# Performance work log

Measured on AMD Instinct MI355X. Metric: run time of the kernel, lower is better.

Reference implementation:

```python
import jax, jax.numpy as jnp
import numpy as np

_N = 262144  # horizon
_n = 64      # state dim
_m = 32      # observation dim


def setup_inputs() -> dict:
    key = jax.random.key(0)
    k1, k2, k3, k4 = jax.random.split(key, 4)
    # Scale so the closed-loop matrix M = A - L H is stable (spectral radius < 1);
    # otherwise the 262k-step recurrence overflows fp32.
    A = jax.random.normal(k1, (_n, _n), jnp.float32) * (0.7 / np.sqrt(_n))
    H = jax.random.normal(k2, (_m, _n), jnp.float32) * (1.0 / np.sqrt(_n))
    L = jax.random.normal(k3, (_n, _m), jnp.float32) * (0.1 / np.sqrt(_m))
    y = jax.random.normal(k4, (_m, _N), jnp.float32)
    return {"y": y, "A": A, "H": H, "L": L, "N": _N}


def reference(y, A, H, L, N):
    # xhat[k+1] = A xhat[k] + L (y[:,k] - H xhat[:,k]) = (A - L H) xhat[k] + L y[:,k]
    # yhat[:,k] = H xhat[:,k],  xhat[0] = 0
    M = A - L @ H  # (n, n) closed-loop transition
    x0 = jnp.zeros((A.shape[0],), dtype=A.dtype)

    def step(x, yk):
        yhat_k = H @ x          # emitted BEFORE the update (matches loop order)
        x_next = M @ x + L @ yk
        return x_next, yhat_k

    _, yhat = jax.lax.scan(step, x0, y.T[:N])  # yhat: (N, m)
    return yhat.T  # (m, N)
```

## Files before the change

### kernel.cpp

```cpp
#include <hip/hip_runtime.h>
#include <hip/hip_bf16.h>


#define NSTEP 262144
#define T 16
#define CCH (NSTEP / T)
#define KDIM (64 + 32 * T)
#define MOUT (32 * T)
#define NBLK 128
#define SB (CCH / NBLK)

typedef _Float16 f16;
typedef _Float16 f16x4 __attribute__((ext_vector_type(4)));
typedef _Float16 f16x8 __attribute__((ext_vector_type(8)));
typedef float f32x4 __attribute__((ext_vector_type(4)));


#define OFF_ZH 0
#define SZ_ZH  (CCH * KDIM / 2)
#define OFF_VT (OFF_ZH + SZ_ZH)
#define SZ_VT  (CCH * 64)
#define OFF_MP (OFF_VT + SZ_VT)
#define SZ_MP  (8 * 4096)
#define OFF_BO (OFF_MP + SZ_MP)
#define SZ_BO  (MOUT * KDIM / 2)
#define OFF_GC (OFF_BO + SZ_BO)
#define SZ_GC  (64 * 512 / 2)
#define OFF_FB (OFF_GC + SZ_GC)
#define SZ_FB  (16 * 2048)
#define OFF_GB (OFF_FB + SZ_FB)
#define SZ_GB  (16 * 2048)
#define OFF_KD (OFF_GB + SZ_GB)
#define SZ_KD  (15 * 1024)
#define OFF_W  (OFF_KD + SZ_KD)
#define OFF_XB (OFF_W + NBLK * 64)

__device__ __forceinline__ void mm128(const float* __restrict__ X,
                                      const float* __restrict__ Y,
                                      float* __restrict__ D,
                                      float* __restrict__ gdst,
                                      const int tid) {
  const int i0 = (tid >> 4) * 8, j0 = (tid & 15) * 4;
  float acc[8][4] = {};
  for (int k0 = 0; k0 < 64; k0 += 4) {
    float4 yc[4];
#pragma unroll
    for (int kk = 0; kk < 4; ++kk)
      yc[kk] = *reinterpret_cast<const float4*>(&Y[(k0 + kk) * 68 + j0]);
#pragma unroll
    for (int r = 0; r < 8; ++r) {
      const float4 xr = *reinterpret_cast<const float4*>(&X[(i0 + r) * 68 + k0]);
      const float xs[4] = {xr.x, xr.y, xr.z, xr.w};
#pragma unroll
      for (int kk = 0; kk < 4; ++kk) {
        acc[r][0] = fmaf(xs[kk], yc[kk].x, acc[r][0]);
        acc[r][1] = fmaf(xs[kk], yc[kk].y, acc[r][1]);
        acc[r][2] = fmaf(xs[kk], yc[kk].z, acc[r][2]);
        acc[r][3] = fmaf(xs[kk], yc[kk].w, acc[r][3]);
      }
    }
  }
#pragma unroll
  for (int r = 0; r < 8; ++r) {
    const float4 v = make_float4(acc[r][0], acc[r][1], acc[r][2], acc[r][3]);
    if (D) *reinterpret_cast<float4*>(&D[(i0 + r) * 68 + j0]) = v;
    if (gdst) *reinterpret_cast<float4*>(&gdst[(i0 + r) * 64 + j0]) = v;
  }
}

__global__ __launch_bounds__(256) void k_pack(const float* __restrict__ y,
                                              f16* __restrict__ Zt) {
  __shared__ f16 Lt[32][264];
  const int tid = threadIdx.x;
  const int ct = blockIdx.x;
  const size_t colbase = (size_t)ct * 256;
#pragma unroll
  for (int v = 0; v < 8; ++v) {
    const int fidx = v * 256 + tid;
    const int row = fidx >> 6, col4 = fidx & 63;
    const float4 w = *reinterpret_cast<const float4*>(y + (size_t)row * NSTEP + colbase + col4 * 4);
    f16x4 h = {(f16)w.x, (f16)w.y, (f16)w.z, (f16)w.w};
    *reinterpret_cast<f16x4*>(&Lt[row][col4 * 4]) = h;
  }
  __syncthreads();
#pragma unroll
  for (int v = 0; v < 4; ++v) {
    const int s = v * 256 + tid;
    const int l = s & 15, lg = (s >> 4) & 3, t = s >> 6;
    f16x8 hv;
#pragma unroll
    for (int e = 0; e < 8; ++e) hv[e] = Lt[lg * 8 + e][l * 16 + t];
    *reinterpret_cast<f16x8*>(Zt + ((size_t)(ct * 18 + 2 + t) * 64 + lg * 16 + l) * 8) = hv;
  }
}

__global__ __launch_bounds__(128) void k_p1(const float* __restrict__ A,
                                            const float* __restrict__ H,
                                            const float* __restrict__ L,
                                            float* __restrict__ MP,
                                            float* __restrict__ Fb,
                                            float* __restrict__ Gb) {
  __shared__ __align__(16) float S0[64 * 68], S1[64 * 68], S2[64 * 68];
  const int tid = threadIdx.x;
  for (int e = tid; e < 512; e += 128) {
    const float4 v = reinterpret_cast<const float4*>(H)[e];
    const int q = e >> 4, j = (e & 15) << 2;
    *reinterpret_cast<float4*>(&S0[q * 68 + j]) = v;
  }
  for (int e = tid; e < 512; e += 128) {
    const float4 v = reinterpret_cast<const float4*>(L)[e];
    const int i = e >> 3, q = (e & 7) << 2;
    S1[(q + 0) * 68 + i] = v.x;
    S1[(q + 1) * 68 + i] = v.y;
    S1[(q + 2) * 68 + i] = v.z;
    S1[(q + 3) * 68 + i] = v.w;
  }
  for (int e = tid; e < 512; e += 128) {
    reinterpret_cast<float4*>(Fb)[e] = reinterpret_cast<const float4*>(H)[e];
    reinterpret_cast<float4*>(Gb)[e] = reinterpret_cast<const float4*>(L)[e];
  }
  __syncthreads();
  {
    const int i0 = (tid >> 4) * 8, j0 = (tid & 15) * 4;
    float acc[8][4];
#pragma unroll
    for (int r = 0; r < 8; ++r) {
      const float4 a = *reinterpret_cast<const float4*>(&A[(i0 + r) * 64 + j0]);
      acc[r][0] = a.x; acc[r][1] = a.y; acc[r][2] = a.z; acc[r][3] = a.w;
    }
    for (int q = 0; q < 32; ++q) {
      const float4 hq = *reinterpret_cast<const float4*>(&S0[q * 68 + j0]);
      const float4 l0 = *reinterpret_cast<const float4*>(&S1[q * 68 + i0]);
      const float4 l1 = *reinterpret_cast<const float4*>(&S1[q * 68 + i0 + 4]);
      const float ls[8] = {l0.x, l0.y, l0.z, l0.w, l1.x, l1.y, l1.z, l1.w};
#pragma unroll
      for (int r = 0; r < 8; ++r) {
        acc[r][0] = fmaf(-ls[r], hq.x, acc[r][0]);
        acc[r][1] = fmaf(-ls[r], hq.y, acc[r][1]);
        acc[r][2] = fmaf(-ls[r], hq.z, acc[r][2]);
        acc[r][3] = fmaf(-ls[r], hq.w, acc[r][3]);
      }
    }
    __syncthreads();
#pragma unroll
    for (int r = 0; r < 8; ++r) {
      const float4 v = make_float4(acc[r][0], acc[r][1], acc[r][2], acc[r][3]);
      *reinterpret_cast<float4*>(&S2[(i0 + r) * 68 + j0]) = v;
      *reinterpret_cast<float4*>(&MP[(i0 + r) * 64 + j0]) = v;
    }
  }
  __syncthreads();
  mm128(S2, S2, S0, MP + 1 * 4096, tid); __syncthreads();
  mm128(S0, S2, nullptr, MP + 6 * 4096, tid); __syncthreads();
  mm128(S0, S0, S1, MP + 2 * 4096, tid); __syncthreads();
  mm128(S1, S1, S0, MP + 3 * 4096, tid); __syncthreads();
  mm128(S1, S0, nullptr, MP + 7 * 4096, tid); __syncthreads();
  mm128(S0, S0, nullptr, MP + 4 * 4096, tid);
}

__global__ __launch_bounds__(256) void k_fg(const float* __restrict__ MP,
                                            float* __restrict__ Fb,
                                            float* __restrict__ Gb,
                                            const int phase) {
  const int tid = threadIdx.x;
  const int nHalf = phase ? 12 : 3;
  const int half = blockIdx.x / nHalf, r = blockIdx.x % nHalf;
  int src, dst, msl;
  if (phase == 0) { src = 0; dst = r + 1; msl = (r == 0) ? 0 : (r == 1) ? 1 : 6; }
  else { const int b = r / 4 + 1, s = r % 4; src = s; dst = 4 * b + s;
         msl = (b == 1) ? 2 : (b == 2) ? 3 : 7; }
  const float* __restrict__ Mx = MP + msl * 4096;
  if (half == 0) {
    const int j = tid & 63, ih = tid >> 6;
    const float* Fs = Fb + src * 2048;
    float* Fd = Fb + dst * 2048;
#pragma unroll
    for (int u = 0; u < 8; ++u) {
      const int i = ih * 8 + u;
      float acc = 0.f;
#pragma unroll 8
      for (int q = 0; q < 64; ++q) acc = fmaf(Fs[i * 64 + q], Mx[q * 64 + j], acc);
      Fd[i * 64 + j] = acc;
    }
  } else {
    const int q = tid & 31, ih = tid >> 5;
    const float* Gs = Gb + src * 2048;
    float* Gd = Gb + dst * 2048;
#pragma unroll
    for (int u = 0; u < 8; ++u) {
      const int i = ih * 8 + u;
      float acc = 0.f;
#pragma unroll 8
      for (int p = 0; p < 64; ++p) acc = fmaf(Mx[i * 64 + p], Gs[p * 32 + q], acc);
      Gd[i * 32 + q] = acc;
    }
  }
}

__global__ __launch_bounds__(256) void k_kd(const float* __restrict__ Fb,
                                            const float* __restrict__ L,
                                            float* __restrict__ Kd) {
  const int o = blockIdx.x * 256 + threadIdx.x;
  const int d = o >> 10, i = (o >> 5) & 31, q = o & 31;
  float acc = 0.f;
#pragma unroll 8
  for (int j = 0; j < 64; ++j) acc = fmaf(Fb[d * 2048 + i * 64 + j], L[j * 32 + q], acc);
  Kd[o] = acc;
}

__global__ __launch_bounds__(256) void k_asm(const float* __restrict__ Fb,
                                             const float* __restrict__ Gb,
                                             const float* __restrict__ Kd,
                                             f16* __restrict__ BOt,
                                             f16* __restrict__ GCt) {
  const int sid = blockIdx.x * 256 + threadIdx.x;
  if (sid < 512 * 72) {
    const int l = sid & 15, lg = (sid >> 4) & 3;
    const int t18 = sid >> 6;
    const int mt = t18 / 18, ks = t18 - mt * 18;
    const int i = mt, t = l;
    const int k0 = ks * 32 + lg * 8;
    f16x8 hv;
    if (k0 + 7 < 64) {
#pragma unroll
      for (int e = 0; e < 8; ++e) hv[e] = (f16)Fb[t * 2048 + i * 64 + k0 + e];
    } else {
      const int kk = k0 - 64;
      const int s = kk >> 5, q0 = kk & 31;
      if (s < t) {
        const int d = t - 1 - s;
#pragma unroll
        for (int e = 0; e < 8; ++e) hv[e] = (f16)Kd[d * 1024 + i * 32 + q0 + e];
      } else {
#pragma unroll
        for (int e = 0; e < 8; ++e) hv[e] = (f16)0.f;
      }
    }
    *reinterpret_cast<f16x8*>(BOt + (size_t)sid * 8) = hv;
  } else {
    const int sid2 = sid - 512 * 72;
    if (sid2 < 4096) {
      const int l = sid2 & 15, lg = (sid2 >> 4) & 3;
      const int t16 = sid2 >> 6;
      const int jt = t16 >> 4, ks = t16 & 15;
      const int j = jt * 16 + l;
      const int ii = lg * 8;
      f16x8 hv;
#pragma unroll
      for (int e = 0; e < 8; ++e) hv[e] = (f16)Gb[(15 - ks) * 2048 + j * 32 + ii + e];
      *reinterpret_cast<f16x8*>(GCt + (size_t)sid2 * 8) = hv;
    }
  }
}

template <int MODE>
__global__ __launch_bounds__(256) void k_mfma(const f16* __restrict__ At,
                                              const f16* __restrict__ Bt,
                                              float* __restrict__ outp,
                                              float* __restrict__ MPow) {
  if (MODE == 0 && blockIdx.x == CCH / 128) {
    __shared__ __align__(16) float C0[64 * 68], C1[64 * 68];
    const int tid2 = threadIdx.x;
    const float* M16 = MPow + 4 * 4096;
    for (int e = tid2; e < 4096; e += 256)
      C0[(e >> 6) * 68 + (e & 63)] = M16[e];
    __syncthreads();
    float* cur = C0;
    float* nxt = C1;
    for (int s = 0; s < 7; ++s) {
      if (tid2 < 128)
        mm128(cur, cur, nxt, (s == 6) ? (MPow + 5 * 4096) : nullptr, tid2);
      __syncthreads();
      float* t = cur; cur = nxt; nxt = t;
    }
    return;
  }
  constexpr int KSTEPS = MODE ? 18 : 16;
  constexpr int AKS0 = MODE ? 0 : 2;
  constexpr int KSB = MODE ? 18 : 16;
  const int tid = threadIdx.x;
  const int wave = tid >> 6, lane = tid & 63;
  const int l15 = lane & 15, lg = lane >> 4;
  const int nn0 = blockIdx.x * 128;
  const int ct0 = blockIdx.x * 8 + wave * 2;
  const int bt0 = MODE ? blockIdx.y * 4 : 0;
  const int laneoff = (lg * 16 + l15) * 8;
  f32x4 acc[2][4] = {};
#pragma unroll 2
  for (int su = 0; su < KSTEPS; ++su) {
    const f16x8 a0 = *reinterpret_cast<const f16x8*>(At + (size_t)((ct0 + 0) * 18 + AKS0 + su) * 512 + laneoff);
    const f16x8 a1 = *reinterpret_cast<const f16x8*>(At + (size_t)((ct0 + 1) * 18 + AKS0 + su) * 512 + laneoff);
#pragma unroll
    for (int bf = 0; bf < 4; ++bf) {
      const f16x8 b = *reinterpret_cast<const f16x8*>(Bt + (size_t)((bt0 + bf) * KSB + su) * 512 + laneoff);
      acc[0][bf] = __builtin_amdgcn_mfma_f32_16x16x32_f16(a0, b, acc[0][bf], 0, 0, 0);
      acc[1][bf] = __builtin_amdgcn_mfma_f32_16x16x32_f16(a1, b, acc[1][bf], 0, 0, 0);
    }
  }
#pragma unroll
  for (int af = 0; af < 2; ++af)
#pragma unroll
    for (int bf = 0; bf < 4; ++bf)
#pragma unroll
      for (int rg = 0; rg < 4; ++rg) {
        const int c = nn0 + wave * 32 + af * 16 + lg * 4 + rg;
        const int mm = bt0 * 16 + bf * 16 + l15;
        if (MODE) {
          outp[(size_t)(mm >> 4) * NSTEP + (size_t)c * 16 + (mm & 15)] = acc[af][bf][rg];
        } else {
          outp[(size_t)c * 64 + mm] = acc[af][bf][rg];
        }
      }
}

__device__ __forceinline__ float lane_bcast(float v, int l) {
  return __uint_as_float(__builtin_amdgcn_readlane(__float_as_uint(v), l));
}

__device__ __forceinline__ float matvec_dot(const float* __restrict__ Prow, float x) {
  float a0 = 0.f, a1 = 0.f, a2 = 0.f, a3 = 0.f;
#pragma unroll
  for (int j = 0; j < 16; ++j) {
    a0 = fmaf(Prow[j +  0], lane_bcast(x, j +  0), a0);
    a1 = fmaf(Prow[j + 16], lane_bcast(x, j + 16), a1);
    a2 = fmaf(Prow[j + 32], lane_bcast(x, j + 32), a2);
    a3 = fmaf(Prow[j + 48], lane_bcast(x, j + 48), a3);
  }
  return (a0 + a1) + (a2 + a3);
}

__device__ __forceinline__ void stage_lds(const float* __restrict__ g,
                                          float* __restrict__ lds,
                                          int n, int lane) {
  const int iters = n >> 8;
  for (int r = 0; r < iters; r += 8) {
    float4 tmp[8];
#pragma unroll
    for (int u = 0; u < 8; ++u)
      tmp[u] = *reinterpret_cast<const float4*>(g + (size_t)(r + u) * 256 + lane * 4);
#pragma unroll
    for (int u = 0; u < 8; ++u)
      *reinterpret_cast<float4*>(lds + (size_t)(r + u) * 256 + lane * 4) = tmp[u];
  }
}

__global__ __launch_bounds__(64, 1) void k_scanA(const float* __restrict__ MP,
                                                 const float* __restrict__ VT,
                                                 float* __restrict__ W) {
  __shared__ float SV[SB * 64];
  const int lane = threadIdx.x;
  const int b = blockIdx.x;
  stage_lds(VT + (size_t)b * SB * 64, SV, SB * 64, lane);
  const float* P = MP + 4 * 4096;
  float Prow[64];
#pragma unroll
  for (int j = 0; j < 64; ++j) Prow[j] = P[lane * 64 + j];
  __syncthreads();
  float x = 0.f;
  for (int s = 0; s < SB; ++s) {
    const float v = SV[s * 64 + lane];
    x = matvec_dot(Prow, x) + v;
  }
  W[b * 64 + lane] = x;
}

__global__ __launch_bounds__(64, 1) void k_scanB(const float* __restrict__ MP,
                                                 const float* __restrict__ W,
                                                 float* __restrict__ XB) {
  __shared__ float SW[NBLK * 64];
  const int lane = threadIdx.x;
  stage_lds(W, SW, NBLK * 64, lane);
  const float* Q = MP + 5 * 4096;
  float Qrow[64];
#pragma unroll
  for (int j = 0; j < 64; ++j) Qrow[j] = Q[lane * 64 + j];
  __syncthreads();
  float x = 0.f;
  for (int b = 0; b < NBLK; ++b) {
    XB[b * 64 + lane] = x;
    const float v = SW[b * 64 + lane];
    x = matvec_dot(Qrow, x) + v;
  }
}

__global__ __launch_bounds__(64, 1) void k_scanC(const float* __restrict__ MP,
                                                 const float* __restrict__ VT,
                                                 const float* __restrict__ XB,
                                                 f16* __restrict__ Zt) {
  __shared__ float SV[SB * 64];
  __shared__ float xt2[SB][68];
  const int lane = threadIdx.x;
  const int b = blockIdx.x;
  stage_lds(VT + (size_t)b * SB * 64, SV, SB * 64, lane);
  const float* P = MP + 4 * 4096;
  float Prow[64];
#pragma unroll
  for (int j = 0; j < 64; ++j) Prow[j] = P[lane * 64 + j];
  float x = XB[b * 64 + lane];
  __syncthreads();
  for (int s = 0; s < SB; ++s) {
    xt2[s][lane] = x;
    const float v = SV[s * 64 + lane];
    x = matvec_dot(Prow, x) + v;
  }
  __syncthreads();
#pragma unroll
  for (int h = 0; h < 2; ++h) {
    const int s = h * 64 + lane;
    const int c = b * SB + s;
    const int ct = c >> 4, l = c & 15;
#pragma unroll
    for (int ks = 0; ks < 2; ++ks)
#pragma unroll
      for (int lg = 0; lg < 4; ++lg) {
        f16x8 hv;
#pragma unroll
        for (int e = 0; e < 8; ++e) hv[e] = (f16)xt2[s][ks * 32 + lg * 8 + e];
        *reinterpret_cast<f16x8*>(Zt + ((size_t)(ct * 18 + ks) * 64 + lg * 16 + l) * 8) = hv;
      }
  }
}

extern "C" void kernel_launch(void* const* d_in, const int* in_sizes, int n_in,
                              void* d_out, int out_size, void* d_ws, size_t ws_size,
                              hipStream_t stream) {
  const float* y = (const float*)d_in[0];
  const float* A = (const float*)d_in[1];
  const float* H = (const float*)d_in[2];
  const float* L = (const float*)d_in[3];
  float* ws = (float*)d_ws;
  f16* Zt   = reinterpret_cast<f16*>(ws + OFF_ZH);
  float* VT = ws + OFF_VT;
  float* MP = ws + OFF_MP;
  f16* BOt  = reinterpret_cast<f16*>(ws + OFF_BO);
  f16* GCt  = reinterpret_cast<f16*>(ws + OFF_GC);
  float* Fb = ws + OFF_FB;
  float* Gb = ws + OFF_GB;
  float* Kd = ws + OFF_KD;
  float* W  = ws + OFF_W;
  float* XB = ws + OFF_XB;
  float* out = (float*)d_out;

  k_pack<<<dim3(CCH / 16), dim3(256), 0, stream>>>(y, Zt);
  k_p1<<<dim3(1), dim3(128), 0, stream>>>(A, H, L, MP, Fb, Gb);
  k_fg<<<dim3(6), dim3(256), 0, stream>>>(MP, Fb, Gb, 0);
  k_fg<<<dim3(24), dim3(256), 0, stream>>>(MP, Fb, Gb, 1);
  k_kd<<<dim3(60), dim3(256), 0, stream>>>(Fb, L, Kd);
  k_asm<<<dim3(160), dim3(256), 0, stream>>>(Fb, Gb, Kd, BOt, GCt);
  k_mfma<0><<<dim3(CCH / 128 + 1, 1), dim3(256), 0, stream>>>(Zt, GCt, VT, MP);
  k_scanA<<<dim3(NBLK), dim3(64), 0, stream>>>(MP, VT, W);
  k_scanB<<<dim3(1), dim3(64), 0, stream>>>(MP, W, XB);
  k_scanC<<<dim3(NBLK), dim3(64), 0, stream>>>(MP, VT, XB, Zt);
  k_mfma<1><<<dim3(CCH / 128, MOUT / 64), dim3(256), 0, stream>>>(Zt, BOt, out, nullptr);
}
```

Before: 292.8 us.

## Fuse small setup and scan kernels using atomic counters and spin waits

Cuts the launch chain from eleven kernels to five. The matrix-power setup becomes an extra block of the pack kernel, and the F/G doubling phases plus assembly are merged into one kernel ordered by global atomic counters and spin-waits. The Kd precompute is folded inline into assembly, and the three scan kernels become one, where the last block to finish runs the serial block-level scan while the others spin. This removes per-launch overhead and idle gaps, but relies on every block being co-resident so the spin waits cannot deadlock, and it repeats the Kd arithmetic per element.

```diff
diff --git a/kernel.cpp b/kernel.cpp
--- a/kernel.cpp
+++ b/kernel.cpp
@@ -30,25 +30,29 @@
 #define SZ_FB  (16 * 2048)
 #define OFF_GB (OFF_FB + SZ_FB)
 #define SZ_GB  (16 * 2048)
-#define OFF_KD (OFF_GB + SZ_GB)
-#define SZ_KD  (15 * 1024)
-#define OFF_W  (OFF_KD + SZ_KD)
+#define OFF_W  (OFF_GB + SZ_GB)
 #define OFF_XB (OFF_W + NBLK * 64)
-
-__device__ __forceinline__ void mm128(const float* __restrict__ X,
+#define OFF_CT (OFF_XB + NBLK * 64)
+
+__device__ __forceinline__ void spin_ge(unsigned* p, unsigned tgt) {
+  while (__hip_atomic_load(p, __ATOMIC_ACQUIRE, __HIP_MEMORY_SCOPE_AGENT) < tgt)
+    __builtin_amdgcn_s_sleep(8);
+}
+
+__device__ __forceinline__ void mm256(const float* __restrict__ X,
                                       const float* __restrict__ Y,
                                       float* __restrict__ D,
                                       float* __restrict__ gdst,
                                       const int tid) {
-  const int i0 = (tid >> 4) * 8, j0 = (tid & 15) * 4;
-  float acc[8][4] = {};
+  const int i0 = (tid >> 4 & 15) * 4, j0 = (tid & 15) * 4;
+  float acc[4][4] = {};
   for (int k0 = 0; k0 < 64; k0 += 4) {
     float4 yc[4];
 #pragma unroll
     for (int kk = 0; kk < 4; ++kk)
       yc[kk] = *reinterpret_cast<const float4*>(&Y[(k0 + kk) * 68 + j0]);
 #pragma unroll
-    for (int r = 0; r < 8; ++r) {
+    for (int r = 0; r < 4; ++r) {
       const float4 xr = *reinterpret_cast<const float4*>(&X[(i0 + r) * 68 + k0]);
       const float xs[4] = {xr.x, xr.y, xr.z, xr.w};
 #pragma unroll
@@ -61,17 +65,84 @@
     }
   }
 #pragma unroll
-  for (int r = 0; r < 8; ++r) {
+  for (int r = 0; r < 4; ++r) {
     const float4 v = make_float4(acc[r][0], acc[r][1], acc[r][2], acc[r][3]);
     if (D) *reinterpret_cast<float4*>(&D[(i0 + r) * 68 + j0]) = v;
     if (gdst) *reinterpret_cast<float4*>(&gdst[(i0 + r) * 64 + j0]) = v;
   }
 }
 
-__global__ __launch_bounds__(256) void k_pack(const float* __restrict__ y,
-                                              f16* __restrict__ Zt) {
-  __shared__ f16 Lt[32][264];
+__global__ __launch_bounds__(256) void k_packp1(const float* __restrict__ y,
+                                                const float* __restrict__ A,
+                                                const float* __restrict__ H,
+                                                const float* __restrict__ L,
+                                                float* __restrict__ MP,
+                                                float* __restrict__ Fb,
+                                                float* __restrict__ Gb,
+                                                f16* __restrict__ Zt,
+                                                unsigned* __restrict__ CT) {
+  __shared__ __align__(16) float SMEM[3 * 64 * 68];
   const int tid = threadIdx.x;
+
+  if (blockIdx.x == CCH / 16) {
+    if (tid == 0) { CT[0] = 0u; CT[1] = 0u; }
+    float* S0 = SMEM;
+    float* S1 = SMEM + 64 * 68;
+    float* S2 = SMEM + 2 * 64 * 68;
+    for (int e = tid; e < 512; e += 256) {
+      const float4 v = reinterpret_cast<const float4*>(H)[e];
+      const int q = e >> 4, j = (e & 15) << 2;
+      *reinterpret_cast<float4*>(&S0[q * 68 + j]) = v;
+      reinterpret_cast<float4*>(Fb)[e] = v;
+    }
+    for (int e = tid; e < 512; e += 256) {
+      const float4 v = reinterpret_cast<const float4*>(L)[e];
+      const int i = e >> 3, q = (e & 7) << 2;
+      S1[(q + 0) * 68 + i] = v.x;
+      S1[(q + 1) * 68 + i] = v.y;
+      S1[(q + 2) * 68 + i] = v.z;
+      S1[(q + 3) * 68 + i] = v.w;
+      reinterpret_cast<float4*>(Gb)[e] = v;
+    }
+    __syncthreads();
+    {
+      const int i0 = (tid >> 4) * 4, j0 = (tid & 15) * 4;
+      float acc[4][4];
+#pragma unroll
+      for (int r = 0; r < 4; ++r) {
+        const float4 a = *reinterpret_cast<const float4*>(&A[(i0 + r) * 64 + j0]);
+        acc[r][0] = a.x; acc[r][1] = a.y; acc[r][2] = a.z; acc[r][3] = a.w;
+      }
+      for (int q = 0; q < 32; ++q) {
+        const float4 hq = *reinterpret_cast<const float4*>(&S0[q * 68 + j0]);
+        const float4 lv = *reinterpret_cast<const float4*>(&S1[q * 68 + i0]);
+        const float ls[4] = {lv.x, lv.y, lv.z, lv.w};
+#pragma unroll
+        for (int r = 0; r < 4; ++r) {
+          acc[r][0] = fmaf(-ls[r], hq.x, acc[r][0]);
+          acc[r][1] = fmaf(-ls[r], hq.y, acc[r][1]);
+          acc[r][2] = fmaf(-ls[r], hq.z, acc[r][2]);
+          acc[r][3] = fmaf(-ls[r], hq.w, acc[r][3]);
+        }
+      }
+      __syncthreads();
+#pragma unroll
+      for (int r = 0; r < 4; ++r) {
+        const float4 v = make_float4(acc[r][0], acc[r][1], acc[r][2], acc[r][3]);
+        *reinterpret_cast<float4*>(&S2[(i0 + r) * 68 + j0]) = v;
+        *reinterpret_cast<float4*>(&MP[(i0 + r) * 64 + j0]) = v;
+      }
+    }
+    __syncthreads();
+    mm256(S2, S2, S0, MP + 1 * 4096, tid); __syncthreads();
+    mm256(S0, S2, nullptr, MP + 6 * 4096, tid); __syncthreads();
+    mm256(S0, S0, S1, MP + 2 * 4096, tid); __syncthreads();
+    mm256(S1, S1, S2, MP + 3 * 4096, tid); __syncthreads();
+    mm256(S1, S2, nullptr, MP + 7 * 4096, tid); __syncthreads();
+    mm256(S2, S2, nullptr, MP + 4 * 4096, tid);
+    return;
+  }
+  f16* Lt = reinterpret_cast<f16*>(SMEM);
   const int ct = blockIdx.x;
   const size_t colbase = (size_t)ct * 256;
 #pragma unroll
@@ -80,7 +151,7 @@
     const int row = fidx >> 6, col4 = fidx & 63;
     const float4 w = *reinterpret_cast<const float4*>(y + (size_t)row * NSTEP + colbase + col4 * 4);
     f16x4 h = {(f16)w.x, (f16)w.y, (f16)w.z, (f16)w.w};
-    *reinterpret_cast<f16x4*>(&Lt[row][col4 * 4]) = h;
+    *reinterpret_cast<f16x4*>(&Lt[row * 264 + col4 * 4]) = h;
   }
   __syncthreads();
 #pragma unroll
@@ -89,131 +160,66 @@
     const int l = s & 15, lg = (s >> 4) & 3, t = s >> 6;
     f16x8 hv;
 #pragma unroll
-    for (int e = 0; e < 8; ++e) hv[e] = Lt[lg * 8 + e][l * 16 + t];
+    for (int e = 0; e < 8; ++e) hv[e] = Lt[(lg * 8 + e) * 264 + l * 16 + t];
     *reinterpret_cast<f16x8*>(Zt + ((size_t)(ct * 18 + 2 + t) * 64 + lg * 16 + l) * 8) = hv;
   }
 }
 
-__global__ __launch_bounds__(128) void k_p1(const float* __restrict__ A,
-                                            const float* __restrict__ H,
-                                            const float* __restrict__ L,
-                                            float* __restrict__ MP,
-                                            float* __restrict__ Fb,
-                                            float* __restrict__ Gb) {
-  __shared__ __align__(16) float S0[64 * 68], S1[64 * 68], S2[64 * 68];
+__global__ __launch_bounds__(256) void k_prep(const float* __restrict__ L,
+                                              const float* __restrict__ MP,
+                                              float* __restrict__ Fb,
+                                              float* __restrict__ Gb,
+                                              f16* __restrict__ BOt,
+                                              f16* __restrict__ GCt,
+                                              unsigned* __restrict__ CT) {
   const int tid = threadIdx.x;
-  for (int e = tid; e < 512; e += 128) {
-    const float4 v = reinterpret_cast<const float4*>(H)[e];
-    const int q = e >> 4, j = (e & 15) << 2;
-    *reinterpret_cast<float4*>(&S0[q * 68 + j]) = v;
-  }
-  for (int e = tid; e < 512; e += 128) {
-    const float4 v = reinterpret_cast<const float4*>(L)[e];
-    const int i = e >> 3, q = (e & 7) << 2;
-    S1[(q + 0) * 68 + i] = v.x;
-    S1[(q + 1) * 68 + i] = v.y;
-    S1[(q + 2) * 68 + i] = v.z;
-    S1[(q + 3) * 68 + i] = v.w;
-  }
-  for (int e = tid; e < 512; e += 128) {
-    reinterpret_cast<float4*>(Fb)[e] = reinterpret_cast<const float4*>(H)[e];
-    reinterpret_cast<float4*>(Gb)[e] = reinterpret_cast<const float4*>(L)[e];
-  }
+  const int blk = blockIdx.x;
+
+  if (blk < 30) {
+    const int phase = (blk >= 6);
+    const int bb = phase ? blk - 6 : blk;
+    const int nHalf = phase ? 12 : 3;
+    const int half = bb / nHalf, r = bb % nHalf;
+    int src, dst, msl;
+    if (!phase) { src = 0; dst = r + 1; msl = (r == 0) ? 0 : (r == 1) ? 1 : 6; }
+    else { const int b2 = r / 4 + 1, s = r % 4; src = s; dst = 4 * b2 + s;
+           msl = (b2 == 1) ? 2 : (b2 == 2) ? 3 : 7; }
+    if (phase) { if (tid == 0) spin_ge(CT + 0, 6u); __syncthreads(); }
+    const float* __restrict__ Mx = MP + msl * 4096;
+    if (half == 0) {
+      const int j = tid & 63, ih = tid >> 6;
+      const float* Fs = Fb + src * 2048;
+      float* Fd = Fb + dst * 2048;
+#pragma unroll
+      for (int u = 0; u < 8; ++u) {
+        const int i = ih * 8 + u;
+        float acc = 0.f;
+#pragma unroll 8
+        for (int q = 0; q < 64; ++q) acc = fmaf(Fs[i * 64 + q], Mx[q * 64 + j], acc);
+        Fd[i * 64 + j] = acc;
+      }
+    } else {
+      const int q = tid & 31, ih = tid >> 5;
+      const float* Gs = Gb + src * 2048;
+      float* Gd = Gb + dst * 2048;
+#pragma unroll
+      for (int u = 0; u < 8; ++u) {
+        const int i = ih * 8 + u;
+        float acc = 0.f;
+#pragma unroll 8
+        for (int p = 0; p < 64; ++p) acc = fmaf(Mx[i * 64 + p], Gs[p * 32 + q], acc);
+        Gd[i * 32 + q] = acc;
+      }
+    }
+    __syncthreads();
+    if (tid == 0)
+      __hip_atomic_fetch_add(CT + phase, 1u, __ATOMIC_ACQ_REL, __HIP_MEMORY_SCOPE_AGENT);
+    return;
+  }
+
+  if (tid == 0) spin_ge(CT + 1, 24u);
   __syncthreads();
-  {
-    const int i0 = (tid >> 4) * 8, j0 = (tid & 15) * 4;
-    float acc[8][4];
-#pragma unroll
-    for (int r = 0; r < 8; ++r) {
-      const float4 a = *reinterpret_cast<const float4*>(&A[(i0 + r) * 64 + j0]);
-      acc[r][0] = a.x; acc[r][1] = a.y; acc[r][2] = a.z; acc[r][3] = a.w;
-    }
-    for (int q = 0; q < 32; ++q) {
-      const float4 hq = *reinterpret_cast<const float4*>(&S0[q * 68 + j0]);
-      const float4 l0 = *reinterpret_cast<const float4*>(&S1[q * 68 + i0]);
-      const float4 l1 = *reinterpret_cast<const float4*>(&S1[q * 68 + i0 + 4]);
-      const float ls[8] = {l0.x, l0.y, l0.z, l0.w, l1.x, l1.y, l1.z, l1.w};
-#pragma unroll
-      for (int r = 0; r < 8; ++r) {
-        acc[r][0] = fmaf(-ls[r], hq.x, acc[r][0]);
-        acc[r][1] = fmaf(-ls[r], hq.y, acc[r][1]);
-        acc[r][2] = fmaf(-ls[r], hq.z, acc[r][2]);
-        acc[r][3] = fmaf(-ls[r], hq.w, acc[r][3]);
-      }
-    }
-    __syncthreads();
-#pragma unroll
-    for (int r = 0; r < 8; ++r) {
-      const float4 v = make_float4(acc[r][0], acc[r][1], acc[r][2], acc[r][3]);
-      *reinterpret_cast<float4*>(&S2[(i0 + r) * 68 + j0]) = v;
-      *reinterpret_cast<float4*>(&MP[(i0 + r) * 64 + j0]) = v;
-    }
-  }
-  __syncthreads();
-  mm128(S2, S2, S0, MP + 1 * 4096, tid); __syncthreads();
-  mm128(S0, S2, nullptr, MP + 6 * 4096, tid); __syncthreads();
-  mm128(S0, S0, S1, MP + 2 * 4096, tid); __syncthreads();
-  mm128(S1, S1, S0, MP + 3 * 4096, tid); __syncthreads();
-  mm128(S1, S0, nullptr, MP + 7 * 4096, tid); __syncthreads();
-  mm128(S0, S0, nullptr, MP + 4 * 4096, tid);
-}
-
-__global__ __launch_bounds__(256) void k_fg(const float* __restrict__ MP,
-                                            float* __restrict__ Fb,
-                                            float* __restrict__ Gb,
-                                            const int phase) {
-  const int tid = threadIdx.x;
-  const int nHalf = phase ? 12 : 3;
-  const int half = blockIdx.x / nHalf, r = blockIdx.x % nHalf;
-  int src, dst, msl;
-  if (phase == 0) { src = 0; dst = r + 1; msl = (r == 0) ? 0 : (r == 1) ? 1 : 6; }
-  else { const int b = r / 4 + 1, s = r % 4; src = s; dst = 4 * b + s;
-         msl = (b == 1) ? 2 : (b == 2) ? 3 : 7; }
-  const float* __restrict__ Mx = MP + msl * 4096;
-  if (half == 0) {
-    const int j = tid & 63, ih = tid >> 6;
-    const float* Fs = Fb + src * 2048;
-    float* Fd = Fb + dst * 2048;
-#pragma unroll
-    for (int u = 0; u < 8; ++u) {
-      const int i = ih * 8 + u;
-      float acc = 0.f;
-#pragma unroll 8
-      for (int q = 0; q < 64; ++q) acc = fmaf(Fs[i * 64 + q], Mx[q * 64 + j], acc);
-      Fd[i * 64 + j] = acc;
-    }
-  } else {
-    const int q = tid & 31, ih = tid >> 5;
-    const float* Gs = Gb + src * 2048;
-    float* Gd = Gb + dst * 2048;
-#pragma unroll
-    for (int u = 0; u < 8; ++u) {
-      const int i = ih * 8 + u;
-      float acc = 0.f;
-#pragma unroll 8
-      for (int p = 0; p < 64; ++p) acc = fmaf(Mx[i * 64 + p], Gs[p * 32 + q], acc);
-      Gd[i * 32 + q] = acc;
-    }
-  }
-}
-
-__global__ __launch_bounds__(256) void k_kd(const float* __restrict__ Fb,
-                                            const float* __restrict__ L,
-                                            float* __restrict__ Kd) {
-  const int o = blockIdx.x * 256 + threadIdx.x;
-  const int d = o >> 10, i = (o >> 5) & 31, q = o & 31;
-  float acc = 0.f;
-#pragma unroll 8
-  for (int j = 0; j < 64; ++j) acc = fmaf(Fb[d * 2048 + i * 64 + j], L[j * 32 + q], acc);
-  Kd[o] = acc;
-}
-
-__global__ __launch_bounds__(256) void k_asm(const float* __restrict__ Fb,
-                                             const float* __restrict__ Gb,
-                                             const float* __restrict__ Kd,
-                                             f16* __restrict__ BOt,
-                                             f16* __restrict__ GCt) {
-  const int sid = blockIdx.x * 256 + threadIdx.x;
+  const int sid = (blk - 30) * 256 + tid;
   if (sid < 512 * 72) {
     const int l = sid & 15, lg = (sid >> 4) & 3;
     const int t18 = sid >> 6;
@@ -229,8 +235,19 @@
       const int s = kk >> 5, q0 = kk & 31;
       if (s < t) {
         const int d = t - 1 - s;
-#pragma unroll
-        for (int e = 0; e < 8; ++e) hv[e] = (f16)Kd[d * 1024 + i * 32 + q0 + e];
+        const float* Frow = Fb + d * 2048 + i * 64;
+        float kv[8] = {};
+        for (int j = 0; j < 64; ++j) {
+          const float f = Frow[j];
+          const float4 l0 = *reinterpret_cast<const float4*>(L + j * 32 + q0);
+          const float4 l1 = *reinterpret_cast<const float4*>(L + j * 32 + q0 + 4);
+          kv[0] = fmaf(f, l0.x, kv[0]); kv[1] = fmaf(f, l0.y, kv[1]);
+          kv[2] = fmaf(f, l0.z, kv[2]); kv[3] = fmaf(f, l0.w, kv[3]);
+          kv[4] = fmaf(f, l1.x, kv[4]); kv[5] = fmaf(f, l1.y, kv[5]);
+          kv[6] = fmaf(f, l1.z, kv[6]); kv[7] = fmaf(f, l1.w, kv[7]);
+        }
+#pragma unroll
+        for (int e = 0; e < 8; ++e) hv[e] = (f16)kv[e];
       } else {
 #pragma unroll
         for (int e = 0; e < 8; ++e) hv[e] = (f16)0.f;
@@ -257,10 +274,12 @@
 __global__ __launch_bounds__(256) void k_mfma(const f16* __restrict__ At,
                                               const f16* __restrict__ Bt,
                                               float* __restrict__ outp,
-                                              float* __restrict__ MPow) {
+                                              float* __restrict__ MPow,
+                                              unsigned* __restrict__ CT) {
   if (MODE == 0 && blockIdx.x == CCH / 128) {
     __shared__ __align__(16) float C0[64 * 68], C1[64 * 68];
     const int tid2 = threadIdx.x;
+    if (tid2 == 0) { CT[2] = 0u; CT[3] = 0u; }
     const float* M16 = MPow + 4 * 4096;
     for (int e = tid2; e < 4096; e += 256)
       C0[(e >> 6) * 68 + (e & 63)] = M16[e];
@@ -268,8 +287,7 @@
     float* cur = C0;
     float* nxt = C1;
     for (int s = 0; s < 7; ++s) {
-      if (tid2 < 128)
-        mm128(cur, cur, nxt, (s == 6) ? (MPow + 5 * 4096) : nullptr, tid2);
+      mm256(cur, cur, nxt, (s == 6) ? (MPow + 5 * 4096) : nullptr, tid2);
       __syncthreads();
       float* t = cur; cur = nxt; nxt = t;
     }
@@ -344,50 +362,14 @@
   }
 }
 
-__global__ __launch_bounds__(64, 1) void k_scanA(const float* __restrict__ MP,
-                                                 const float* __restrict__ VT,
-                                                 float* __restrict__ W) {
+__global__ __launch_bounds__(64, 1) void k_scan(const float* __restrict__ MP,
+                                                const float* __restrict__ VT,
+                                                float* __restrict__ W,
+                                                float* __restrict__ XB,
+                                                unsigned* __restrict__ CT,
+                                                f16* __restrict__ Zt) {
   __shared__ float SV[SB * 64];
-  const int lane = threadIdx.x;
-  const int b = blockIdx.x;
-  stage_lds(VT + (size_t)b * SB * 64, SV, SB * 64, lane);
-  const float* P = MP + 4 * 4096;
-  float Prow[64];
-#pragma unroll
-  for (int j = 0; j < 64; ++j) Prow[j] = P[lane * 64 + j];
-  __syncthreads();
-  float x = 0.f;
-  for (int s = 0; s < SB; ++s) {
-    const float v = SV[s * 64 + lane];
-    x = matvec_dot(Prow, x) + v;
-  }
-  W[b * 64 + lane] = x;
-}
-
-__global__ __launch_bounds__(64, 1) void k_scanB(const float* __restrict__ MP,
-                                                 const float* __restrict__ W,
-                                                 float* __restrict__ XB) {
   __shared__ float SW[NBLK * 64];
-  const int lane = threadIdx.x;
-  stage_lds(W, SW, NBLK * 64, lane);
-  const float* Q = MP + 5 * 4096;
-  float Qrow[64];
-#pragma unroll
-  for (int j = 0; j < 64; ++j) Qrow[j] = Q[lane * 64 + j];
-  __syncthreads();
-  float x = 0.f;
-  for (int b = 0; b < NBLK; ++b) {
-    XB[b * 64 + lane] = x;
-    const float v = SW[b * 64 + lane];
-    x = matvec_dot(Qrow, x) + v;
-  }
-}
-
-__global__ __launch_bounds__(64, 1) void k_scanC(const float* __restrict__ MP,
-                                                 const float* __restrict__ VT,
-                                                 const float* __restrict__ XB,
-                                                 f16* __restrict__ Zt) {
-  __shared__ float SV[SB * 64];
   __shared__ float xt2[SB][68];
   const int lane = threadIdx.x;
   const int b = blockIdx.x;
@@ -396,12 +378,38 @@
   float Prow[64];
 #pragma unroll
   for (int j = 0; j < 64; ++j) Prow[j] = P[lane * 64 + j];
-  float x = XB[b * 64 + lane];
   __syncthreads();
+  float x = 0.f;
+  for (int s = 0; s < SB; ++s) x = matvec_dot(Prow, x) + SV[s * 64 + lane];
+  W[b * 64 + lane] = x;
+  unsigned old = 0u;
+  if (lane == 0)
+    old = __hip_atomic_fetch_add(CT + 2, 1u, __ATOMIC_ACQ_REL, __HIP_MEMORY_SCOPE_AGENT);
+  old = (unsigned)__shfl((int)old, 0);
+  if (old == NBLK - 1) {
+    stage_lds(W, SW, NBLK * 64, lane);
+    const float* Q = MP + 5 * 4096;
+    float Qrow[64];
+#pragma unroll
+    for (int j = 0; j < 64; ++j) Qrow[j] = Q[lane * 64 + j];
+    __syncthreads();
+    float x2 = 0.f;
+    for (int b2 = 0; b2 < NBLK; ++b2) {
+      XB[b2 * 64 + lane] = x2;
+      x2 = matvec_dot(Qrow, x2) + SW[b2 * 64 + lane];
+    }
+    if (lane == 0)
+      __hip_atomic_store(CT + 3, 1u, __ATOMIC_RELEASE, __HIP_MEMORY_SCOPE_AGENT);
+  }
+  if (lane == 0) {
+    while (__hip_atomic_load(CT + 3, __ATOMIC_ACQUIRE, __HIP_MEMORY_SCOPE_AGENT) == 0u)
+      __builtin_amdgcn_s_sleep(8);
+  }
+  __syncthreads();
+  x = XB[b * 64 + lane];
   for (int s = 0; s < SB; ++s) {
     xt2[s][lane] = x;
-    const float v = SV[s * 64 + lane];
-    x = matvec_dot(Prow, x) + v;
+    x = matvec_dot(Prow, x) + SV[s * 64 + lane];
   }
   __syncthreads();
 #pragma unroll
@@ -436,20 +444,14 @@
   f16* GCt  = reinterpret_cast<f16*>(ws + OFF_GC);
   float* Fb = ws + OFF_FB;
   float* Gb = ws + OFF_GB;
-  float* Kd = ws + OFF_KD;
   float* W  = ws + OFF_W;
   float* XB = ws + OFF_XB;
+  unsigned* CT = reinterpret_cast<unsigned*>(ws + OFF_CT);
   float* out = (float*)d_out;
 
-  k_pack<<<dim3(CCH / 16), dim3(256), 0, stream>>>(y, Zt);
-  k_p1<<<dim3(1), dim3(128), 0, stream>>>(A, H, L, MP, Fb, Gb);
-  k_fg<<<dim3(6), dim3(256), 0, stream>>>(MP, Fb, Gb, 0);
-  k_fg<<<dim3(24), dim3(256), 0, stream>>>(MP, Fb, Gb, 1);
-  k_kd<<<dim3(60), dim3(256), 0, stream>>>(Fb, L, Kd);
-  k_asm<<<dim3(160), dim3(256), 0, stream>>>(Fb, Gb, Kd, BOt, GCt);
-  k_mfma<0><<<dim3(CCH / 128 + 1, 1), dim3(256), 0, stream>>>(Zt, GCt, VT, MP);
-  k_scanA<<<dim3(NBLK), dim3(64), 0, stream>>>(MP, VT, W);
-  k_scanB<<<dim3(1), dim3(64), 0, stream>>>(MP, W, XB);
-  k_scanC<<<dim3(NBLK), dim3(64), 0, stream>>>(MP, VT, XB, Zt);
-  k_mfma<1><<<dim3(CCH / 128, MOUT / 64), dim3(256), 0, stream>>>(Zt, BOt, out, nullptr);
-}
+  k_packp1<<<dim3(CCH / 16 + 1), dim3(256), 0, stream>>>(y, A, H, L, MP, Fb, Gb, Zt, CT);
+  k_prep<<<dim3(190), dim3(256), 0, stream>>>(L, MP, Fb, Gb, BOt, GCt, CT);
+  k_mfma<0><<<dim3(CCH / 128 + 1, 1), dim3(256), 0, stream>>>(Zt, GCt, VT, MP, CT);
+  k_scan<<<dim3(NBLK), dim3(64), 0, stream>>>(MP, VT, W, XB, CT, Zt);
+  k_mfma<1><<<dim3(CCH / 128, MOUT / 64), dim3(256), 0, stream>>>(Zt, BOt, out, MP, CT);
+}
```

Measured after the change: 321.2 us. 1.1x slower.
